# Kernel optimization log

Hardware: AMD Instinct MI355X
Metric: run time of the kernel (lower is better)

## Reference

```python
import jax, jax.numpy as jnp
import numpy as np

H = 8
DH = 64  # attention_head_size
HID = 512
NEG = -90000000000.0

def _lin(x, w, b):
    return x @ w + b

def _tfs(x):  # [N, HID] -> [H, N, DH]
    n = x.shape[0]
    return x.reshape(n, H, DH).transpose(1, 0, 2)

def _cross(q, ck, v, cv, mask, dw, db):
    # q: [H,N,DH], ck/cv: [H,M,DH], v: [H,N,DH], mask: [N,M]
    s = jnp.einsum('hnd,hmd->hnm', q, ck)
    s = s * mask[None, :, :] / jnp.sqrt(jnp.asarray(DH, s.dtype))
    s = jnp.where(s == 0.0, NEG, s)  # faithful zero->-inf hack
    p = jax.nn.softmax(s, axis=-1)
    ctx = v + jnp.einsum('hnm,hmd->hnd', p, cv)  # residual add of raw value
    n = ctx.shape[1]
    ctx = ctx.transpose(1, 0, 2).reshape(n, H * DH)
    return _lin(ctx, dw, db)

def setup_inputs() -> dict:
    key = jax.random.key(0)
    ks = jax.random.split(key, 24)
    N1, N2, D1 = 4096, 4096, 300
    d = {}
    d['h_head'] = jax.random.normal(ks[0], (N1, D1), jnp.float32)
    d['h_tail'] = jax.random.normal(ks[1], (N2, HID), jnp.float32)
    d['batch_head'] = jnp.sort(jax.random.randint(ks[2], (N1,), 0, 64))
    d['batch_tail'] = jnp.sort(jax.random.randint(ks[3], (N2,), 0, 64))
    def w(k, i, o):
        return jax.random.normal(k, (i, o), jnp.float32) / np.sqrt(i)
    d['map_w'] = w(ks[4], D1, HID); d['map_b'] = jnp.zeros((HID,), jnp.float32)
    names = ['q1', 'k1', 'v1', 'q2', 'k2', 'v2', 'd1', 'd2']
    for i, nm in enumerate(names):
        d[nm + '_w'] = w(ks[5 + i], HID, HID)
        d[nm + '_b'] = jnp.zeros((HID,), jnp.float32)
    return d

def reference(h_head, h_tail, batch_head, batch_tail,
              map_w, map_b,
              q1_w, q1_b, k1_w, k1_b, v1_w, v1_b,
              q2_w, q2_b, k2_w, k2_b, v2_w, v2_b,
              d1_w, d1_b, d2_w, d2_b):
    hh = _lin(h_head, map_w, map_b)  # n_dim1 != n_dim2 -> map
    q_h = _tfs(_lin(hh, q1_w, q1_b))
    k_h = _tfs(_lin(hh, k1_w, k1_b))
    v_h = _tfs(_lin(hh, v1_w, v1_b))
    q_t = _tfs(_lin(h_tail, q2_w, q2_b))
    k_t = _tfs(_lin(h_tail, k2_w, k2_b))
    v_t = _tfs(_lin(h_tail, v2_w, v2_b))
    mask = (batch_head[:, None] == batch_tail[None, :]).astype(jnp.float32)
    out_head = _cross(q_h, k_t, v_h, v_t, mask, d1_w, d1_b)
    out_tail = _cross(q_t, k_h, v_t, v_h, mask.T, d2_w, d2_b)
    return (out_head, out_tail)
```

## Files before the change

### kernel.cpp

```cpp
#include <hip/hip_runtime.h>
#include <hip/hip_bf16.h>
#include <math.h>


typedef __bf16 bf16x8 __attribute__((ext_vector_type(8)));
typedef float  f32x4  __attribute__((ext_vector_type(4)));

#define HID 512
#define NTOK 4096

#define AS1(p) ((const __attribute__((address_space(1))) void*)(p))
#define AS3(p) ((__attribute__((address_space(3))) void*)(p))

__global__ __launch_bounds__(256) void prep_inputs(
    const float* __restrict__ h_head, const float* __restrict__ h_tail,
    const int* __restrict__ bh, const int* __restrict__ bt,
    __bf16* __restrict__ hh_bf, __bf16* __restrict__ ht_bf,
    int* __restrict__ ranges)
{
    const int q = blockIdx.x, z = blockIdx.z, tid = threadIdx.x;

    if (z == 0) {
        if (q == 0 && tid < 128) {
            int b = tid & 63;
            const int* arr = (tid < 64) ? bh : bt;
            int base = (tid < 64) ? 0 : 128;
            int lo = 0, hi = NTOK;
            while (lo < hi) { int mid = (lo + hi) >> 1; if (arr[mid] < b) lo = mid + 1; else hi = mid; }
            int start = lo;
            lo = 0; hi = NTOK;
            while (lo < hi) { int mid = (lo + hi) >> 1; if (arr[mid] <= b) lo = mid + 1; else hi = mid; }
            ranges[base + b] = start;
            ranges[base + 64 + b] = lo;
        }
        for (int idx = tid; idx < 8 * 40; idx += 256) {
            int r   = q * 8 + idx / 40;
            int col = (idx % 40) * 8;
            bf16x8 v;
            if (col + 8 <= 300) {
                float4 f0 = *(const float4*)&h_head[(size_t)r * 300 + col];
                float4 f1 = *(const float4*)&h_head[(size_t)r * 300 + col + 4];
                v[0]=(__bf16)f0.x; v[1]=(__bf16)f0.y; v[2]=(__bf16)f0.z; v[3]=(__bf16)f0.w;
                v[4]=(__bf16)f1.x; v[5]=(__bf16)f1.y; v[6]=(__bf16)f1.z; v[7]=(__bf16)f1.w;
            } else if (col < 300) {
                float4 f0 = *(const float4*)&h_head[(size_t)r * 300 + col];
                v[0]=(__bf16)f0.x; v[1]=(__bf16)f0.y; v[2]=(__bf16)f0.z; v[3]=(__bf16)f0.w;
                v[4]=(__bf16)0.f; v[5]=(__bf16)0.f; v[6]=(__bf16)0.f; v[7]=(__bf16)0.f;
            } else {
                #pragma unroll
                for (int j = 0; j < 8; ++j) v[j] = (__bf16)0.f;
            }
            *(bf16x8*)&hh_bf[(size_t)r * 320 + col] = v;
        }
    } else {
        for (int idx = tid; idx < 8 * 64; idx += 256) {
            int r   = q * 8 + (idx >> 6);
            int col = (idx & 63) * 8;
            float4 f0 = *(const float4*)&h_tail[(size_t)r * 512 + col];
            float4 f1 = *(const float4*)&h_tail[(size_t)r * 512 + col + 4];
            bf16x8 v;
            v[0]=(__bf16)f0.x; v[1]=(__bf16)f0.y; v[2]=(__bf16)f0.z; v[3]=(__bf16)f0.w;
            v[4]=(__bf16)f1.x; v[5]=(__bf16)f1.y; v[6]=(__bf16)f1.z; v[7]=(__bf16)f1.w;
            *(bf16x8*)&ht_bf[(size_t)r * 512 + col] = v;
        }
    }
}

struct TransJobs {
    const float* src[9];
    __bf16*      dst[9];
    int          K[9];
    int          ldT[9];
};

__global__ __launch_bounds__(256) void transpose_weights(TransJobs tj) {
    const int z = blockIdx.z;
    const float* src = tj.src[z];
    __bf16* dst = tj.dst[z];
    const int K = tj.K[z], ldT = tj.ldT[z];
    const int tk = blockIdx.y * 64;
    const int tn = blockIdx.x * 64;
    if (tk >= ldT) return;

    __shared__ __bf16 T[64][72];
    const int tid = threadIdx.x;
    const int r0 = tid >> 4;
    const int c0 = (tid & 15) * 4;
    #pragma unroll
    for (int i = 0; i < 4; ++i) {
        int k = tk + r0 + i * 16;
        float4 v = (k < K) ? *(const float4*)&src[(size_t)k * 512 + tn + c0]
                           : float4{0.f, 0.f, 0.f, 0.f};
        T[r0 + i * 16][c0 + 0] = (__bf16)v.x;
        T[r0 + i * 16][c0 + 1] = (__bf16)v.y;
        T[r0 + i * 16][c0 + 2] = (__bf16)v.z;
        T[r0 + i * 16][c0 + 3] = (__bf16)v.w;
    }
    __syncthreads();

    const int n  = tid >> 2;
    const int kk = (tid & 3) * 16;
    bf16x8 o0, o1;
    #pragma unroll
    for (int j = 0; j < 8; ++j) { o0[j] = T[kk + j][n]; o1[j] = T[kk + 8 + j][n]; }
    __bf16* dp = dst + (size_t)(tn + n) * ldT + tk + kk;
    *(bf16x8*)dp       = o0;
    *(bf16x8*)(dp + 8) = o1;
}

struct GemmJobs {
    const __bf16* A[4];
    const __bf16* W[4];
    const float*  bias[4];
    void*         C[4];
    int           Kp[4];
};

template <typename TC>
__global__ __launch_bounds__(256) void gemm128(GemmJobs jobs) {
    __shared__ __align__(16) __bf16 As[2][4096];
    __shared__ __align__(16) __bf16 Bs[2][4096];

    const int z = blockIdx.z;
    const __bf16* A    = jobs.A[z];
    const __bf16* W    = jobs.W[z];
    const float*  bias = jobs.bias[z];
    TC*           C    = (TC*)jobs.C[z];
    const int     Kp   = jobs.Kp[z];

    const int tid  = threadIdx.x;
    const int wave = tid >> 6;
    const int lane = tid & 63;
    const int quad = lane >> 4;
    const int l16  = lane & 15;
    const int wy   = wave >> 1;
    const int wx   = wave & 1;
    const int rowBase = blockIdx.y * 128;
    const int colBase = blockIdx.x * 128;

    const int s_row = tid >> 2;
    const int s_kc  = ((tid & 3) ^ ((s_row >> 1) & 3)) * 8;

    const __bf16* gA = A + (size_t)(rowBase + s_row) * Kp + s_kc;
    const __bf16* gB = W + (size_t)(colBase + s_row) * Kp + s_kc;
    const int waveOff = wave * 512;

    f32x4 acc[4][4] = {};
    const int nk = Kp >> 5;

    __builtin_amdgcn_global_load_lds(AS1(gA),                   AS3(&As[0][waveOff]),        16, 0, 0);
    __builtin_amdgcn_global_load_lds(AS1(gA + (size_t)64 * Kp), AS3(&As[0][2048 + waveOff]), 16, 0, 0);
    __builtin_amdgcn_global_load_lds(AS1(gB),                   AS3(&Bs[0][waveOff]),        16, 0, 0);
    __builtin_amdgcn_global_load_lds(AS1(gB + (size_t)64 * Kp), AS3(&Bs[0][2048 + waveOff]), 16, 0, 0);

    for (int i = 0; i < nk; ++i) {
        const int cur = i & 1;
        __syncthreads();

        if (i + 1 < nk) {
            const int kt = (i + 1) * 32;
            const int nx = cur ^ 1;
            __builtin_amdgcn_global_load_lds(AS1(gA + kt),                   AS3(&As[nx][waveOff]),        16, 0, 0);
            __builtin_amdgcn_global_load_lds(AS1(gA + kt + (size_t)64 * Kp), AS3(&As[nx][2048 + waveOff]), 16, 0, 0);
            __builtin_amdgcn_global_load_lds(AS1(gB + kt),                   AS3(&Bs[nx][waveOff]),        16, 0, 0);
            __builtin_amdgcn_global_load_lds(AS1(gB + kt + (size_t)64 * Kp), AS3(&Bs[nx][2048 + waveOff]), 16, 0, 0);
        }

        bf16x8 ar[4], br[4];
        #pragma unroll
        for (int ii = 0; ii < 4; ++ii) {
            const int ra = wy * 64 + ii * 16 + l16;
            ar[ii] = *(const bf16x8*)&As[cur][ra * 32 + ((quad ^ ((ra >> 1) & 3)) << 3)];
        }
        #pragma unroll
        for (int jj = 0; jj < 4; ++jj) {
            const int rb = wx * 64 + jj * 16 + l16;
            br[jj] = *(const bf16x8*)&Bs[cur][rb * 32 + ((quad ^ ((rb >> 1) & 3)) << 3)];
        }
        #pragma unroll
        for (int ii = 0; ii < 4; ++ii)
            #pragma unroll
            for (int jj = 0; jj < 4; ++jj)
                acc[ii][jj] = __builtin_amdgcn_mfma_f32_16x16x32_bf16(ar[ii], br[jj], acc[ii][jj], 0, 0, 0);
    }

    #pragma unroll
    for (int jj = 0; jj < 4; ++jj) {
        int col = colBase + wx * 64 + jj * 16 + l16;
        float bv = bias[col];
        #pragma unroll
        for (int ii = 0; ii < 4; ++ii) {
            #pragma unroll
            for (int r = 0; r < 4; ++r) {
                int row = rowBase + wy * 64 + ii * 16 + quad * 4 + r;
                C[(size_t)row * HID + col] = (TC)(acc[ii][jj][r] + bv);
            }
        }
    }
}

__global__ __launch_bounds__(256) void attn_mfma(
    const __bf16* __restrict__ Q0, const __bf16* __restrict__ K0,
    const __bf16* __restrict__ Vr0, const __bf16* __restrict__ Vc0,
    const __bf16* __restrict__ Q1, const __bf16* __restrict__ K1,
    const __bf16* __restrict__ Vr1, const __bf16* __restrict__ Vc1,
    const int* __restrict__ ranges,
    __bf16* __restrict__ O0, __bf16* __restrict__ O1,
    int Nq, int Nk)
{
    __shared__ __align__(16) __bf16 Qs[64][72];
    __shared__ __align__(16) __bf16 Ks[64][72];
    __shared__ __align__(16) __bf16 Vt[64][72];
    __shared__ __align__(16) __bf16 Ps[64][72];

    const int z = blockIdx.z;
    const __bf16* Q    = z ? Q1 : Q0;
    const __bf16* Kg   = z ? K1 : K0;
    const __bf16* Vres = z ? Vr1 : Vr0;
    const __bf16* Vctx = z ? Vc1 : Vc0;
    __bf16* Out        = z ? O1 : O0;
    const int* qstart  = z ? ranges + 128 : ranges;
    const int* qend    = z ? ranges + 192 : ranges + 64;
    const int* kstart  = z ? ranges       : ranges + 128;
    const int* kend    = z ? ranges + 64  : ranges + 192;

    const int h = blockIdx.x, b = blockIdx.y;
    const int qs = qstart[b], qe = qend[b];
    const int ts = kstart[b], te = kend[b];
    const int nq = qe - qs, nk = te - ts;
    if (nq <= 0) return;

    const int tid  = threadIdx.x;
    const int wave = tid >> 6;
    const int lane = tid & 63;
    const int quad = lane >> 4;
    const int l16  = lane & 15;
    const int srow = tid >> 2;
    const int scol = (tid & 3) * 16;

    if (nk <= 0) {
        float* meanv = (float*)Qs;
        if (tid < 64) {
            float s = 0.f;
            for (int m = 0; m < Nk; ++m)
                s += (float)Vctx[(size_t)m * HID + h * 64 + tid];
            meanv[tid] = s / (float)Nk;
        }
        __syncthreads();
        int d = tid & 63;
        for (int r = qs + (tid >> 6); r < qe; r += 4) {
            size_t off = (size_t)r * HID + h * 64 + d;
            Out[off] = (__bf16)((float)Vres[off] + meanv[d]);
        }
        return;
    }

    for (int qc = 0; qc < nq; qc += 64) {
        __syncthreads();
        {
            int qg = min(qs + qc + srow, Nq - 1);
            const __bf16* src = Q + (size_t)qg * HID + h * 64 + scol;
            *(bf16x8*)&Qs[srow][scol]     = *(const bf16x8*)src;
            *(bf16x8*)&Qs[srow][scol + 8] = *(const bf16x8*)(src + 8);
        }
        __syncthreads();
        bf16x8 aq0 = *(const bf16x8*)&Qs[wave * 16 + l16][quad * 8];
        bf16x8 aq1 = *(const bf16x8*)&Qs[wave * 16 + l16][32 + quad * 8];

        f32x4 O[4] = {};
        float Mx[4], L[4];
        #pragma unroll
        for (int r = 0; r < 4; ++r) { Mx[r] = -__builtin_inff(); L[r] = 0.f; }

        for (int kc = 0; kc < nk; kc += 64) {
            __syncthreads();
            {
                int kg = min(ts + kc + srow, Nk - 1);
                const __bf16* ksrc = Kg + (size_t)kg * HID + h * 64 + scol;
                *(bf16x8*)&Ks[srow][scol]     = *(const bf16x8*)ksrc;
                *(bf16x8*)&Ks[srow][scol + 8] = *(const bf16x8*)(ksrc + 8);
                const __bf16* vsrc = Vctx + (size_t)kg * HID + h * 64 + scol;
                bf16x8 v0 = *(const bf16x8*)vsrc;
                bf16x8 v1 = *(const bf16x8*)(vsrc + 8);
                #pragma unroll
                for (int j = 0; j < 8; ++j) {
                    Vt[scol + j][srow]     = v0[j];
                    Vt[scol + 8 + j][srow] = v1[j];
                }
            }
            __syncthreads();

            f32x4 S[4] = {};
            #pragma unroll
            for (int c = 0; c < 4; ++c) {
                bf16x8 bk0 = *(const bf16x8*)&Ks[c * 16 + l16][quad * 8];
                bf16x8 bk1 = *(const bf16x8*)&Ks[c * 16 + l16][32 + quad * 8];
                S[c] = __builtin_amdgcn_mfma_f32_16x16x32_bf16(aq0, bk0, S[c], 0, 0, 0);
                S[c] = __builtin_amdgcn_mfma_f32_16x16x32_bf16(aq1, bk1, S[c], 0, 0, 0);
            }

            #pragma unroll
            for (int c = 0; c < 4; ++c) {
                bool valid = (ts + kc + c * 16 + l16) < te;
                #pragma unroll
                for (int r = 0; r < 4; ++r)
                    S[c][r] = valid ? S[c][r] * 0.125f : -__builtin_inff();
            }

            float cm[4], ps[4], alpha[4];
            #pragma unroll
            for (int r = 0; r < 4; ++r) {
                float v = fmaxf(fmaxf(S[0][r], S[1][r]), fmaxf(S[2][r], S[3][r]));
                v = fmaxf(v, __shfl_xor(v, 1, 64));
                v = fmaxf(v, __shfl_xor(v, 2, 64));
                v = fmaxf(v, __shfl_xor(v, 4, 64));
                v = fmaxf(v, __shfl_xor(v, 8, 64));
                cm[r] = v;
            }
            #pragma unroll
            for (int r = 0; r < 4; ++r) {
                float nM = fmaxf(Mx[r], cm[r]);
                alpha[r] = __expf(Mx[r] - nM);
                Mx[r] = nM;
                ps[r] = 0.f;
            }
            #pragma unroll
            for (int c = 0; c < 4; ++c)
                #pragma unroll
                for (int r = 0; r < 4; ++r) {
                    float p = __expf(S[c][r] - Mx[r]);
                    S[c][r] = p;
                    ps[r] += p;
                }
            #pragma unroll
            for (int r = 0; r < 4; ++r) {
                float v = ps[r];
                v += __shfl_xor(v, 1, 64);
                v += __shfl_xor(v, 2, 64);
                v += __shfl_xor(v, 4, 64);
                v += __shfl_xor(v, 8, 64);
                L[r] = L[r] * alpha[r] + v;
            }
            #pragma unroll
            for (int c = 0; c < 4; ++c)
                #pragma unroll
                for (int r = 0; r < 4; ++r)
                    O[c][r] *= alpha[r];

            #pragma unroll
            for (int c = 0; c < 4; ++c)
                #pragma unroll
                for (int r = 0; r < 4; ++r)
                    Ps[wave * 16 + quad * 4 + r][c * 16 + l16] = (__bf16)S[c][r];
            __syncthreads();

            bf16x8 ap0 = *(const bf16x8*)&Ps[wave * 16 + l16][quad * 8];
            bf16x8 ap1 = *(const bf16x8*)&Ps[wave * 16 + l16][32 + quad * 8];
            #pragma unroll
            for (int c = 0; c < 4; ++c) {
                bf16x8 bv0 = *(const bf16x8*)&Vt[c * 16 + l16][quad * 8];
                bf16x8 bv1 = *(const bf16x8*)&Vt[c * 16 + l16][32 + quad * 8];
                O[c] = __builtin_amdgcn_mfma_f32_16x16x32_bf16(ap0, bv0, O[c], 0, 0, 0);
                O[c] = __builtin_amdgcn_mfma_f32_16x16x32_bf16(ap1, bv1, O[c], 0, 0, 0);
            }
        }

        #pragma unroll
        for (int c = 0; c < 4; ++c) {
            int d = h * 64 + c * 16 + l16;
            #pragma unroll
            for (int r = 0; r < 4; ++r) {
                int qrow = qs + qc + wave * 16 + quad * 4 + r;
                if (qrow < qe) {
                    size_t off = (size_t)qrow * HID + d;
                    Out[off] = (__bf16)((float)Vres[off] + O[c][r] / L[r]);
                }
            }
        }
    }
}

extern "C" void kernel_launch(void* const* d_in, const int* in_sizes, int n_in,
                              void* d_out, int out_size, void* d_ws, size_t ws_size,
                              hipStream_t stream) {
    (void)in_sizes; (void)n_in; (void)out_size; (void)ws_size;

    const float* h_head = (const float*)d_in[0];
    const float* h_tail = (const float*)d_in[1];
    const int* batch_head = (const int*)d_in[2];
    const int* batch_tail = (const int*)d_in[3];
    const float* map_w = (const float*)d_in[4];
    const float* map_b = (const float*)d_in[5];
    const float* q1_w = (const float*)d_in[6];
    const float* q1_b = (const float*)d_in[7];
    const float* k1_w = (const float*)d_in[8];
    const float* k1_b = (const float*)d_in[9];
    const float* v1_w = (const float*)d_in[10];
    const float* v1_b = (const float*)d_in[11];
    const float* q2_w = (const float*)d_in[12];
    const float* q2_b = (const float*)d_in[13];
    const float* k2_w = (const float*)d_in[14];
    const float* k2_b = (const float*)d_in[15];
    const float* v2_w = (const float*)d_in[16];
    const float* v2_b = (const float*)d_in[17];
    const float* d1_w = (const float*)d_in[18];
    const float* d1_b = (const float*)d_in[19];
    const float* d2_w = (const float*)d_in[20];
    const float* d2_b = (const float*)d_in[21];

    float* out = (float*)d_out;

    const size_t SZ = (size_t)NTOK * HID;
    char* ws = (char*)d_ws;
    int* ranges = (int*)ws;
    __bf16* hh   = (__bf16*)(ws + 1024);
    __bf16* qh   = hh  + SZ;
    __bf16* kh   = qh  + SZ;
    __bf16* vh   = kh  + SZ;
    __bf16* qt   = vh  + SZ;
    __bf16* kt   = qt  + SZ;
    __bf16* vt   = kt  + SZ;
    __bf16* ctxh = vt  + SZ;
    __bf16* ctxt = ctxh + SZ;
    __bf16* mapT = ctxt + SZ;
    __bf16* q1T  = mapT + 512 * 320;
    __bf16* k1T  = q1T + 512 * 512;
    __bf16* v1T  = k1T + 512 * 512;
    __bf16* q2T  = v1T + 512 * 512;
    __bf16* k2T  = q2T + 512 * 512;
    __bf16* v2T  = k2T + 512 * 512;
    __bf16* d1T  = v2T + 512 * 512;
    __bf16* d2T  = d1T + 512 * 512;
    __bf16* hh_bf = d2T + 512 * 512;
    __bf16* ht_bf = hh_bf + (size_t)NTOK * 320;

    prep_inputs<<<dim3(512, 1, 2), dim3(256), 0, stream>>>(
        h_head, h_tail, batch_head, batch_tail, hh_bf, ht_bf, ranges);

    TransJobs tj;
    tj.src[0] = map_w; tj.dst[0] = mapT; tj.K[0] = 300; tj.ldT[0] = 320;
    const float* wsrc[8] = {q1_w, k1_w, v1_w, q2_w, k2_w, v2_w, d1_w, d2_w};
    __bf16* wdst[8] = {q1T, k1T, v1T, q2T, k2T, v2T, d1T, d2T};
    for (int i = 0; i < 8; ++i) {
        tj.src[i + 1] = wsrc[i]; tj.dst[i + 1] = wdst[i];
        tj.K[i + 1] = 512; tj.ldT[i + 1] = 512;
    }
    transpose_weights<<<dim3(8, 8, 9), dim3(256), 0, stream>>>(tj);

    {
        GemmJobs j;
        j.A[0] = hh_bf; j.W[0] = mapT; j.bias[0] = map_b; j.C[0] = hh; j.Kp[0] = 320;
        j.A[1] = ht_bf; j.W[1] = q2T; j.bias[1] = q2_b; j.C[1] = qt; j.Kp[1] = 512;
        j.A[2] = ht_bf; j.W[2] = k2T; j.bias[2] = k2_b; j.C[2] = kt; j.Kp[2] = 512;
        j.A[3] = ht_bf; j.W[3] = v2T; j.bias[3] = v2_b; j.C[3] = vt; j.Kp[3] = 512;
        gemm128<__bf16><<<dim3(4, 32, 4), dim3(256), 0, stream>>>(j);
    }
    {
        GemmJobs j;
        j.A[0] = hh; j.W[0] = q1T; j.bias[0] = q1_b; j.C[0] = qh; j.Kp[0] = 512;
        j.A[1] = hh; j.W[1] = k1T; j.bias[1] = k1_b; j.C[1] = kh; j.Kp[1] = 512;
        j.A[2] = hh; j.W[2] = v1T; j.bias[2] = v1_b; j.C[2] = vh; j.Kp[2] = 512;
        j.A[3] = hh; j.W[3] = v1T; j.bias[3] = v1_b; j.C[3] = vh; j.Kp[3] = 512;
        gemm128<__bf16><<<dim3(4, 32, 3), dim3(256), 0, stream>>>(j);
    }

    attn_mfma<<<dim3(8, 64, 2), dim3(256), 0, stream>>>(
        qh, kt, vh, vt,
        qt, kh, vt, vh,
        ranges, ctxh, ctxt, NTOK, NTOK);

    {
        GemmJobs j;
        j.A[0] = ctxh; j.W[0] = d1T; j.bias[0] = d1_b; j.C[0] = out;      j.Kp[0] = 512;
        j.A[1] = ctxt; j.W[1] = d2T; j.bias[1] = d2_b; j.C[1] = out + SZ; j.Kp[1] = 512;
        j.A[2] = ctxt; j.W[2] = d2T; j.bias[2] = d2_b; j.C[2] = out + SZ; j.Kp[2] = 512;
        j.A[3] = ctxt; j.W[3] = d2T; j.bias[3] = d2_b; j.C[3] = out + SZ; j.Kp[3] = 512;
        gemm128<float><<<dim3(4, 32, 2), dim3(256), 0, stream>>>(j);
    }
}
```

Baseline: 187.8 us.

## Fold map projection into head QKV weights and fuse prep kernels

Precomputes the products of the head QKV weights and the map weight (and the folded biases), so the head Q/K/V projections run directly from the 320-wide input instead of first materialising the 512-wide mapped tensor. This removes one full GEMM stage and its dependency, so all six QKV projections run in a single launch. The input conversion, range search, weight transposes and map-weight conversion are merged into one prep kernel. In exchange, a small weight-product GEMM and a serial bias-fold loop are added per call, and the folded weights add an extra bf16 rounding step.

New measurement: 193.8 us. 3.2% more time.

```diff
diff --git a/kernel.cpp b/kernel.cpp
--- a/kernel.cpp
+++ b/kernel.cpp
@@ -12,108 +12,126 @@
 #define AS1(p) ((const __attribute__((address_space(1))) void*)(p))
 #define AS3(p) ((__attribute__((address_space(3))) void*)(p))
 
-__global__ __launch_bounds__(256) void prep_inputs(
-    const float* __restrict__ h_head, const float* __restrict__ h_tail,
-    const int* __restrict__ bh, const int* __restrict__ bt,
-    __bf16* __restrict__ hh_bf, __bf16* __restrict__ ht_bf,
-    int* __restrict__ ranges)
-{
+struct PrepArgs {
+    const float* h_head; const float* h_tail;
+    const int* bh; const int* bt;
+    const float* map_w; const float* map_b;
+    const float* qkvw[3]; const float* qkvb[3];
+    const float* tsrc[8]; __bf16* tdst[8];
+    __bf16* hh_bf; __bf16* ht_bf; __bf16* mapw_bf;
+    float* fb;
+    int* ranges;
+};
+
+__global__ __launch_bounds__(256) void fused_prep(PrepArgs pa) {
     const int q = blockIdx.x, z = blockIdx.z, tid = threadIdx.x;
+    __shared__ __bf16 T[64][72];
 
     if (z == 0) {
         if (q == 0 && tid < 128) {
             int b = tid & 63;
-            const int* arr = (tid < 64) ? bh : bt;
+            const int* arr = (tid < 64) ? pa.bh : pa.bt;
             int base = (tid < 64) ? 0 : 128;
             int lo = 0, hi = NTOK;
             while (lo < hi) { int mid = (lo + hi) >> 1; if (arr[mid] < b) lo = mid + 1; else hi = mid; }
             int start = lo;
             lo = 0; hi = NTOK;
             while (lo < hi) { int mid = (lo + hi) >> 1; if (arr[mid] <= b) lo = mid + 1; else hi = mid; }
-            ranges[base + b] = start;
-            ranges[base + 64 + b] = lo;
+            pa.ranges[base + b] = start;
+            pa.ranges[base + 64 + b] = lo;
         }
         for (int idx = tid; idx < 8 * 40; idx += 256) {
             int r   = q * 8 + idx / 40;
             int col = (idx % 40) * 8;
             bf16x8 v;
             if (col + 8 <= 300) {
-                float4 f0 = *(const float4*)&h_head[(size_t)r * 300 + col];
-                float4 f1 = *(const float4*)&h_head[(size_t)r * 300 + col + 4];
+                float4 f0 = *(const float4*)&pa.h_head[(size_t)r * 300 + col];
+                float4 f1 = *(const float4*)&pa.h_head[(size_t)r * 300 + col + 4];
                 v[0]=(__bf16)f0.x; v[1]=(__bf16)f0.y; v[2]=(__bf16)f0.z; v[3]=(__bf16)f0.w;
                 v[4]=(__bf16)f1.x; v[5]=(__bf16)f1.y; v[6]=(__bf16)f1.z; v[7]=(__bf16)f1.w;
             } else if (col < 300) {
-                float4 f0 = *(const float4*)&h_head[(size_t)r * 300 + col];
+                float4 f0 = *(const float4*)&pa.h_head[(size_t)r * 300 + col];
                 v[0]=(__bf16)f0.x; v[1]=(__bf16)f0.y; v[2]=(__bf16)f0.z; v[3]=(__bf16)f0.w;
                 v[4]=(__bf16)0.f; v[5]=(__bf16)0.f; v[6]=(__bf16)0.f; v[7]=(__bf16)0.f;
             } else {
                 #pragma unroll
                 for (int j = 0; j < 8; ++j) v[j] = (__bf16)0.f;
             }
-            *(bf16x8*)&hh_bf[(size_t)r * 320 + col] = v;
-        }
-    } else {
+            *(bf16x8*)&pa.hh_bf[(size_t)r * 320 + col] = v;
+        }
+    } else if (z == 1) {
         for (int idx = tid; idx < 8 * 64; idx += 256) {
             int r   = q * 8 + (idx >> 6);
             int col = (idx & 63) * 8;
-            float4 f0 = *(const float4*)&h_tail[(size_t)r * 512 + col];
-            float4 f1 = *(const float4*)&h_tail[(size_t)r * 512 + col + 4];
+            float4 f0 = *(const float4*)&pa.h_tail[(size_t)r * 512 + col];
+            float4 f1 = *(const float4*)&pa.h_tail[(size_t)r * 512 + col + 4];
             bf16x8 v;
             v[0]=(__bf16)f0.x; v[1]=(__bf16)f0.y; v[2]=(__bf16)f0.z; v[3]=(__bf16)f0.w;
             v[4]=(__bf16)f1.x; v[5]=(__bf16)f1.y; v[6]=(__bf16)f1.z; v[7]=(__bf16)f1.w;
-            *(bf16x8*)&ht_bf[(size_t)r * 512 + col] = v;
-        }
+            *(bf16x8*)&pa.ht_bf[(size_t)r * 512 + col] = v;
+        }
+    } else if (z == 2) {
+        if (q < 96) {
+            int r   = q * 4 + (tid >> 6);
+            int col = (tid & 63) * 8;
+            bf16x8 v;
+            if (r < 300) {
+                float4 f0 = *(const float4*)&pa.map_w[(size_t)r * 512 + col];
+                float4 f1 = *(const float4*)&pa.map_w[(size_t)r * 512 + col + 4];
+                v[0]=(__bf16)f0.x; v[1]=(__bf16)f0.y; v[2]=(__bf16)f0.z; v[3]=(__bf16)f0.w;
+                v[4]=(__bf16)f1.x; v[5]=(__bf16)f1.y; v[6]=(__bf16)f1.z; v[7]=(__bf16)f1.w;
+            } else {
+                #pragma unroll
+                for (int j = 0; j < 8; ++j) v[j] = (__bf16)0.f;
+            }
+            *(bf16x8*)&pa.mapw_bf[(size_t)r * 512 + col] = v;
+        } else if (q < 102) {
+            int b2 = q - 96;
+            int w  = b2 >> 1;
+            int n  = ((b2 & 1) << 8) + tid;
+            const float* W = pa.qkvw[w];
+            float s = pa.qkvb[w][n];
+            for (int j = 0; j < 512; ++j)
+                s += pa.map_b[j] * W[(size_t)j * 512 + n];
+            pa.fb[w * 512 + n] = s;
+        }
+    } else {
+        if (q >= 64) return;
+        const int jz = z - 3;
+        const float* src = pa.tsrc[jz];
+        __bf16* dst = pa.tdst[jz];
+        const int tk = (q >> 3) * 64;
+        const int tn = (q & 7) * 64;
+        const int r0 = tid >> 4;
+        const int c0 = (tid & 15) * 4;
+        #pragma unroll
+        for (int i = 0; i < 4; ++i) {
+            float4 v = *(const float4*)&src[(size_t)(tk + r0 + i * 16) * 512 + tn + c0];
+            T[r0 + i * 16][c0 + 0] = (__bf16)v.x;
+            T[r0 + i * 16][c0 + 1] = (__bf16)v.y;
+            T[r0 + i * 16][c0 + 2] = (__bf16)v.z;
+            T[r0 + i * 16][c0 + 3] = (__bf16)v.w;
+        }
+        __syncthreads();
+        const int n  = tid >> 2;
+        const int kk = (tid & 3) * 16;
+        bf16x8 o0, o1;
+        #pragma unroll
+        for (int j = 0; j < 8; ++j) { o0[j] = T[kk + j][n]; o1[j] = T[kk + 8 + j][n]; }
+        __bf16* dp = dst + (size_t)(tn + n) * 512 + tk + kk;
+        *(bf16x8*)dp       = o0;
+        *(bf16x8*)(dp + 8) = o1;
     }
 }
 
-struct TransJobs {
-    const float* src[9];
-    __bf16*      dst[9];
-    int          K[9];
-    int          ldT[9];
-};
-
-__global__ __launch_bounds__(256) void transpose_weights(TransJobs tj) {
-    const int z = blockIdx.z;
-    const float* src = tj.src[z];
-    __bf16* dst = tj.dst[z];
-    const int K = tj.K[z], ldT = tj.ldT[z];
-    const int tk = blockIdx.y * 64;
-    const int tn = blockIdx.x * 64;
-    if (tk >= ldT) return;
-
-    __shared__ __bf16 T[64][72];
-    const int tid = threadIdx.x;
-    const int r0 = tid >> 4;
-    const int c0 = (tid & 15) * 4;
-    #pragma unroll
-    for (int i = 0; i < 4; ++i) {
-        int k = tk + r0 + i * 16;
-        float4 v = (k < K) ? *(const float4*)&src[(size_t)k * 512 + tn + c0]
-                           : float4{0.f, 0.f, 0.f, 0.f};
-        T[r0 + i * 16][c0 + 0] = (__bf16)v.x;
-        T[r0 + i * 16][c0 + 1] = (__bf16)v.y;
-        T[r0 + i * 16][c0 + 2] = (__bf16)v.z;
-        T[r0 + i * 16][c0 + 3] = (__bf16)v.w;
-    }
-    __syncthreads();
-
-    const int n  = tid >> 2;
-    const int kk = (tid & 3) * 16;
-    bf16x8 o0, o1;
-    #pragma unroll
-    for (int j = 0; j < 8; ++j) { o0[j] = T[kk + j][n]; o1[j] = T[kk + 8 + j][n]; }
-    __bf16* dp = dst + (size_t)(tn + n) * ldT + tk + kk;
-    *(bf16x8*)dp       = o0;
-    *(bf16x8*)(dp + 8) = o1;
-}
-
 struct GemmJobs {
-    const __bf16* A[4];
-    const __bf16* W[4];
-    const float*  bias[4];
-    void*         C[4];
-    int           Kp[4];
+    const __bf16* A[6];
+    const __bf16* W[6];
+    const float*  bias[6];
+    void*         C[6];
+    int           Kp[6];
+    int           ldC[6];
+    int           Ncol[6];
 };
 
 template <typename TC>
@@ -184,16 +202,20 @@
                 acc[ii][jj] = __builtin_amdgcn_mfma_f32_16x16x32_bf16(ar[ii], br[jj], acc[ii][jj], 0, 0, 0);
     }
 
+    const int ldC  = jobs.ldC[z];
+    const int Ncol = jobs.Ncol[z];
     #pragma unroll
     for (int jj = 0; jj < 4; ++jj) {
         int col = colBase + wx * 64 + jj * 16 + l16;
-        float bv = bias[col];
-        #pragma unroll
-        for (int ii = 0; ii < 4; ++ii) {
-            #pragma unroll
-            for (int r = 0; r < 4; ++r) {
-                int row = rowBase + wy * 64 + ii * 16 + quad * 4 + r;
-                C[(size_t)row * HID + col] = (TC)(acc[ii][jj][r] + bv);
+        if (col < Ncol) {
+            float bv = bias ? bias[col] : 0.f;
+            #pragma unroll
+            for (int ii = 0; ii < 4; ++ii) {
+                #pragma unroll
+                for (int r = 0; r < 4; ++r) {
+                    int row = rowBase + wy * 64 + ii * 16 + quad * 4 + r;
+                    C[(size_t)row * ldC + col] = (TC)(acc[ii][jj][r] + bv);
+                }
             }
         }
     }
@@ -412,9 +434,22 @@
 
     const size_t SZ = (size_t)NTOK * HID;
     char* ws = (char*)d_ws;
-    int* ranges = (int*)ws;
-    __bf16* hh   = (__bf16*)(ws + 1024);
-    __bf16* qh   = hh  + SZ;
+    int* ranges   = (int*)ws;
+    __bf16* hh_bf = (__bf16*)(ws + 1024);
+    __bf16* ht_bf = hh_bf + (size_t)NTOK * 320;
+    __bf16* mapw_bf = ht_bf + SZ;
+    __bf16* q1T  = mapw_bf + 384 * 512;
+    __bf16* k1T  = q1T + 512 * 512;
+    __bf16* v1T  = k1T + 512 * 512;
+    __bf16* q2T  = v1T + 512 * 512;
+    __bf16* k2T  = q2T + 512 * 512;
+    __bf16* v2T  = k2T + 512 * 512;
+    __bf16* d1T  = v2T + 512 * 512;
+    __bf16* d2T  = d1T + 512 * 512;
+    __bf16* FqT  = d2T + 512 * 512;
+    __bf16* FkT  = FqT + 512 * 320;
+    __bf16* FvT  = FkT + 512 * 320;
+    __bf16* qh   = FvT + 512 * 320;
     __bf16* kh   = qh  + SZ;
     __bf16* vh   = kh  + SZ;
     __bf16* qt   = vh  + SZ;
@@ -422,46 +457,43 @@
     __bf16* vt   = kt  + SZ;
     __bf16* ctxh = vt  + SZ;
     __bf16* ctxt = ctxh + SZ;
-    __bf16* mapT = ctxt + SZ;
-    __bf16* q1T  = mapT + 512 * 320;
-    __bf16* k1T  = q1T + 512 * 512;
-    __bf16* v1T  = k1T + 512 * 512;
-    __bf16* q2T  = v1T + 512 * 512;
-    __bf16* k2T  = q2T + 512 * 512;
-    __bf16* v2T  = k2T + 512 * 512;
-    __bf16* d1T  = v2T + 512 * 512;
-    __bf16* d2T  = d1T + 512 * 512;
-    __bf16* hh_bf = d2T + 512 * 512;
-    __bf16* ht_bf = hh_bf + (size_t)NTOK * 320;
-
-    prep_inputs<<<dim3(512, 1, 2), dim3(256), 0, stream>>>(
-        h_head, h_tail, batch_head, batch_tail, hh_bf, ht_bf, ranges);
-
-    TransJobs tj;
-    tj.src[0] = map_w; tj.dst[0] = mapT; tj.K[0] = 300; tj.ldT[0] = 320;
+    float*  fb   = (float*)(ctxt + SZ);
+
+    PrepArgs pa;
+    pa.h_head = h_head; pa.h_tail = h_tail;
+    pa.bh = batch_head; pa.bt = batch_tail;
+    pa.map_w = map_w; pa.map_b = map_b;
+    pa.qkvw[0] = q1_w; pa.qkvw[1] = k1_w; pa.qkvw[2] = v1_w;
+    pa.qkvb[0] = q1_b; pa.qkvb[1] = k1_b; pa.qkvb[2] = v1_b;
     const float* wsrc[8] = {q1_w, k1_w, v1_w, q2_w, k2_w, v2_w, d1_w, d2_w};
     __bf16* wdst[8] = {q1T, k1T, v1T, q2T, k2T, v2T, d1T, d2T};
-    for (int i = 0; i < 8; ++i) {
-        tj.src[i + 1] = wsrc[i]; tj.dst[i + 1] = wdst[i];
-        tj.K[i + 1] = 512; tj.ldT[i + 1] = 512;
-    }
-    transpose_weights<<<dim3(8, 8, 9), dim3(256), 0, stream>>>(tj);
+    for (int i = 0; i < 8; ++i) { pa.tsrc[i] = wsrc[i]; pa.tdst[i] = wdst[i]; }
+    pa.hh_bf = hh_bf; pa.ht_bf = ht_bf; pa.mapw_bf = mapw_bf;
+    pa.fb = fb; pa.ranges = ranges;
+    fused_prep<<<dim3(512, 1, 11), dim3(256), 0, stream>>>(pa);
 
     {
         GemmJobs j;
-        j.A[0] = hh_bf; j.W[0] = mapT; j.bias[0] = map_b; j.C[0] = hh; j.Kp[0] = 320;
-        j.A[1] = ht_bf; j.W[1] = q2T; j.bias[1] = q2_b; j.C[1] = qt; j.Kp[1] = 512;
-        j.A[2] = ht_bf; j.W[2] = k2T; j.bias[2] = k2_b; j.C[2] = kt; j.Kp[2] = 512;
-        j.A[3] = ht_bf; j.W[3] = v2T; j.bias[3] = v2_b; j.C[3] = vt; j.Kp[3] = 512;
-        gemm128<__bf16><<<dim3(4, 32, 4), dim3(256), 0, stream>>>(j);
-    }
+        const __bf16* a3[3] = {q1T, k1T, v1T};
+        __bf16* c3[3] = {FqT, FkT, FvT};
+        for (int i = 0; i < 6; ++i) {
+            int s = i < 3 ? i : 0;
+            j.A[i] = a3[s]; j.W[i] = mapw_bf; j.bias[i] = nullptr;
+            j.C[i] = c3[s]; j.Kp[i] = 512; j.ldC[i] = 320; j.Ncol[i] = 320;
+        }
+        gemm128<__bf16><<<dim3(3, 4, 3), dim3(256), 0, stream>>>(j);
+    }
+
     {
         GemmJobs j;
-        j.A[0] = hh; j.W[0] = q1T; j.bias[0] = q1_b; j.C[0] = qh; j.Kp[0] = 512;
-        j.A[1] = hh; j.W[1] = k1T; j.bias[1] = k1_b; j.C[1] = kh; j.Kp[1] = 512;
-        j.A[2] = hh; j.W[2] = v1T; j.bias[2] = v1_b; j.C[2] = vh; j.Kp[2] = 512;
-        j.A[3] = hh; j.W[3] = v1T; j.bias[3] = v1_b; j.C[3] = vh; j.Kp[3] = 512;
-        gemm128<__bf16><<<dim3(4, 32, 3), dim3(256), 0, stream>>>(j);
+        j.A[0] = hh_bf; j.W[0] = FqT; j.bias[0] = fb;        j.C[0] = qh; j.Kp[0] = 320;
+        j.A[1] = hh_bf; j.W[1] = FkT; j.bias[1] = fb + 512;  j.C[1] = kh; j.Kp[1] = 320;
+        j.A[2] = hh_bf; j.W[2] = FvT; j.bias[2] = fb + 1024; j.C[2] = vh; j.Kp[2] = 320;
+        j.A[3] = ht_bf; j.W[3] = q2T; j.bias[3] = q2_b;      j.C[3] = qt; j.Kp[3] = 512;
+        j.A[4] = ht_bf; j.W[4] = k2T; j.bias[4] = k2_b;      j.C[4] = kt; j.Kp[4] = 512;
+        j.A[5] = ht_bf; j.W[5] = v2T; j.bias[5] = v2_b;      j.C[5] = vt; j.Kp[5] = 512;
+        for (int i = 0; i < 6; ++i) { j.ldC[i] = HID; j.Ncol[i] = HID; }
+        gemm128<__bf16><<<dim3(4, 32, 6), dim3(256), 0, stream>>>(j);
     }
 
     attn_mfma<<<dim3(8, 64, 2), dim3(256), 0, stream>>>(
@@ -471,10 +503,14 @@
 
     {
         GemmJobs j;
-        j.A[0] = ctxh; j.W[0] = d1T; j.bias[0] = d1_b; j.C[0] = out;      j.Kp[0] = 512;
-        j.A[1] = ctxt; j.W[1] = d2T; j.bias[1] = d2_b; j.C[1] = out + SZ; j.Kp[1] = 512;
-        j.A[2] = ctxt; j.W[2] = d2T; j.bias[2] = d2_b; j.C[2] = out + SZ; j.Kp[2] = 512;
-        j.A[3] = ctxt; j.W[3] = d2T; j.bias[3] = d2_b; j.C[3] = out + SZ; j.Kp[3] = 512;
+        for (int i = 0; i < 6; ++i) {
+            int s = i < 2 ? i : 0;
+            j.A[i] = s ? ctxt : ctxh;
+            j.W[i] = s ? d2T : d1T;
+            j.bias[i] = s ? d2_b : d1_b;
+            j.C[i] = s ? (void*)(out + SZ) : (void*)out;
+            j.Kp[i] = 512; j.ldC[i] = HID; j.Ncol[i] = HID;
+        }
         gemm128<float><<<dim3(4, 32, 2), dim3(256), 0, stream>>>(j);
     }
 }
```
